# Kernel tuning notes

Hardware: AMD Instinct MI355X
Metric: run time of the kernel (lower is better)

The kernel has to match this reference:

```python
import jax, jax.numpy as jnp
import numpy as np

D_MODEL = 768
NUM_HEADS = 12
HEAD_DIM = D_MODEL // NUM_HEADS

def setup_inputs() -> dict:
    key = jax.random.key(0)
    ks = jax.random.split(key, 7)
    B, S = 2, 4096
    q = jax.random.normal(ks[0], (B, S, D_MODEL), dtype=jnp.float32)
    k = jax.random.normal(ks[1], (B, S, D_MODEL), dtype=jnp.float32)
    v = jax.random.normal(ks[2], (B, S, D_MODEL), dtype=jnp.float32)
    # nn.Linear(d, d, bias=False): weight [out, in], y = x @ W.T
    s = 1.0 / np.sqrt(D_MODEL)
    W_q = jax.random.uniform(ks[3], (D_MODEL, D_MODEL), jnp.float32, -s, s)
    W_k = jax.random.uniform(ks[4], (D_MODEL, D_MODEL), jnp.float32, -s, s)
    W_v = jax.random.uniform(ks[5], (D_MODEL, D_MODEL), jnp.float32, -s, s)
    W_o = jax.random.uniform(ks[6], (D_MODEL, D_MODEL), jnp.float32, -s, s)
    return {"query": q, "key": k, "value": v,
            "W_q": W_q, "W_k": W_k, "W_v": W_v, "W_o": W_o}

def reference(query, key, value, W_q, W_k, W_v, W_o):
    B, S, _ = query.shape
    H, Dh = NUM_HEADS, HEAD_DIM
    scale = np.sqrt(Dh).astype(np.float32)

    def proj(x, W):  # x [B,S,D] -> [B,H,S,Dh]
        y = jnp.einsum('bsd,ed->bse', x, W)
        return y.reshape(B, S, H, Dh).transpose(0, 2, 1, 3)

    Q = proj(query, W_q)
    K = proj(key, W_k)
    V = proj(value, W_v)
    scores = jnp.einsum('bhqd,bhkd->bhqk', Q, K) / scale
    attn = jax.nn.softmax(scores, axis=-1)  # dropout p=0 -> identity (eval)
    out = jnp.einsum('bhqk,bhkd->bhqd', attn, V)
    out = out.transpose(0, 2, 1, 3).reshape(B, S, H * Dh)
    return jnp.einsum('bsd,ed->bse', out, W_o)
```

## Files before the change

### kernel.cpp

```cpp
#include <hip/hip_runtime.h>

#define D_MODEL 768
#define S_LEN   4096
#define NHEAD   12
#define HDIM    64
#define BATCH   2
#define M_ROWS  (BATCH * S_LEN)

typedef __bf16    bf16x8 __attribute__((ext_vector_type(8)));
typedef float     f32x4  __attribute__((ext_vector_type(4)));
typedef float     f32x16 __attribute__((ext_vector_type(16)));
typedef unsigned  u32x4  __attribute__((ext_vector_type(4)));

#define QSCALE 0.18033688011f

__device__ __forceinline__ unsigned int bfb(float x) {
    return (unsigned int)__builtin_bit_cast(unsigned short, (__bf16)x);
}

__device__ __forceinline__ unsigned cvtpk(float lo, float hi) {
    unsigned r;
    asm("v_cvt_pk_bf16_f32 %0, %1, %2" : "=v"(r) : "v"(lo), "v"(hi));
    return r;
}

__device__ __forceinline__ void gload16(const void* g, const void* l) {
    __builtin_amdgcn_global_load_lds(
        (const __attribute__((address_space(1))) unsigned int*)g,
        (__attribute__((address_space(3))) unsigned int*)l, 16, 0, 0);
}

#define MFMA16(a, b, c) __builtin_amdgcn_mfma_f32_16x16x32_bf16(a, b, c, 0, 0, 0)
#define MFMA32(a, b, c) __builtin_amdgcn_mfma_f32_32x32x16_bf16(a, b, c, 0, 0, 0)

__global__ __launch_bounds__(256)
void cvt_bf16(const float* __restrict__ s0, const float* __restrict__ s1,
              const float* __restrict__ s2, const float* __restrict__ s3,
              __bf16* __restrict__ d0, __bf16* __restrict__ d1,
              __bf16* __restrict__ d2, __bf16* __restrict__ d3, int n) {
    const int z = blockIdx.y;
    const float* s = z == 0 ? s0 : z == 1 ? s1 : z == 2 ? s2 : s3;
    __bf16*      d = z == 0 ? d0 : z == 1 ? d1 : z == 2 ? d2 : d3;
    const size_t i = ((size_t)blockIdx.x * 256 + threadIdx.x) * 8;
    if (i >= (size_t)n) return;
    float4 a = *(const float4*)(s + i);
    float4 b = *(const float4*)(s + i + 4);
    bf16x8 o;
    o[0] = (__bf16)a.x; o[1] = (__bf16)a.y; o[2] = (__bf16)a.z; o[3] = (__bf16)a.w;
    o[4] = (__bf16)b.x; o[5] = (__bf16)b.y; o[6] = (__bf16)b.z; o[7] = (__bf16)b.w;
    *(bf16x8*)(d + i) = o;
}

template <int MODE>
__global__ __launch_bounds__(256)
void mm_bf16(const __bf16* __restrict__ Xb, const __bf16* __restrict__ Wb,
             void* __restrict__ C0) {
    __shared__ __align__(16) char lds[16384];
    const int t    = threadIdx.x;
    const int w    = t >> 6;
    const int wr   = w >> 1, wc = w & 1;
    const int lane = t & 63;
    const int q15  = lane & 15;
    const int g    = lane >> 4;
    const int n0   = blockIdx.x * 128;
    const int m0   = blockIdx.y * 128;

    f32x4 acc[4][4];
#pragma unroll
    for (int i = 0; i < 4; i++)
#pragma unroll
        for (int j = 0; j < 4; j++) acc[i][j] = (f32x4){0.f, 0.f, 0.f, 0.f};

    const int srow  = lane >> 2;
    const int sslot = lane & 3;

    for (int k0 = 0; k0 < D_MODEL; k0 += 32) {
        __syncthreads();
#pragma unroll
        for (int j = 0; j < 2; j++) {
            const int lrow = j * 64 + w * 16 + srow;
            const int xs   = (lrow ^ (lrow >> 2)) & 3;
            gload16(Xb + (size_t)(m0 + lrow) * D_MODEL + k0 + ((sslot ^ xs) << 3),
                    lds + j * 4096 + w * 1024);
        }
#pragma unroll
        for (int j = 0; j < 2; j++) {
            const int lrow = j * 64 + w * 16 + srow;
            const int xs   = (lrow ^ (lrow >> 2)) & 3;
            gload16(Wb + (size_t)(n0 + lrow) * D_MODEL + k0 + ((sslot ^ xs) << 3),
                    lds + 8192 + j * 4096 + w * 1024);
        }
        __syncthreads();

        bf16x8 xa[4], wf[4];
#pragma unroll
        for (int mi = 0; mi < 4; mi++) {
            const int r  = wr * 64 + mi * 16 + q15;
            const int sl = g ^ ((r ^ (r >> 2)) & 3);
            xa[mi] = *(const bf16x8*)(lds + r * 64 + sl * 16);
        }
#pragma unroll
        for (int nj = 0; nj < 4; nj++) {
            const int r  = wc * 64 + nj * 16 + q15;
            const int sl = g ^ ((r ^ (r >> 2)) & 3);
            wf[nj] = *(const bf16x8*)(lds + 8192 + r * 64 + sl * 16);
        }
#pragma unroll
        for (int mi = 0; mi < 4; mi++)
#pragma unroll
            for (int nj = 0; nj < 4; nj++)
                acc[mi][nj] = MFMA16(xa[mi], wf[nj], acc[mi][nj]);
    }

#pragma unroll
    for (int mi = 0; mi < 4; mi++) {
#pragma unroll
        for (int nj = 0; nj < 4; nj++) {
            const int n  = n0 + wc * 64 + nj * 16 + q15;
            const int mb = m0 + wr * 64 + mi * 16 + 4 * g;
            if (MODE == 0) {
#pragma unroll
                for (int r = 0; r < 4; r++)
                    ((float*)C0)[(size_t)(mb + r) * D_MODEL + n] = acc[mi][nj][r];
            } else if (MODE == 1) {
                const int h = n >> 6, dh = n & 63;
#pragma unroll
                for (int r = 0; r < 4; r++) {
                    const int m = mb + r, b = m >> 12, s = m & 4095;
                    ((__bf16*)C0)[(((size_t)(b * NHEAD + h)) * S_LEN + s) * HDIM + dh] =
                        (__bf16)(acc[mi][nj][r] * QSCALE);
                }
            } else if (MODE == 2) {
                const int h = n >> 6, dh = n & 63;
#pragma unroll
                for (int r = 0; r < 4; r++) {
                    const int m = mb + r, b = m >> 12, s = m & 4095;
                    ((__bf16*)C0)[(((size_t)(b * NHEAD + h)) * S_LEN + s) * HDIM + dh] =
                        (__bf16)acc[mi][nj][r];
                }
            } else {
                const int h = n >> 6, dh = n & 63;
                const int b = mb >> 12, s = mb & 4095;
                uint2 pk;
                pk.x = bfb(acc[mi][nj][0]) | (bfb(acc[mi][nj][1]) << 16);
                pk.y = bfb(acc[mi][nj][2]) | (bfb(acc[mi][nj][3]) << 16);
                *(uint2*)((__bf16*)C0 +
                    (((size_t)(b * NHEAD + h)) * HDIM + dh) * S_LEN + s) = pk;
            }
        }
    }
}

__global__ __launch_bounds__(256, 2)
void flash_attn(const __bf16* __restrict__ Qb, const char* __restrict__ Kb,
                const char* __restrict__ Vtb, __bf16* __restrict__ Ab) {
    __shared__ __align__(16) char lds[32768];
    const int t    = threadIdx.x;
    const int w    = t >> 6;
    const int lane = t & 63;
    const int q31  = lane & 31;
    const int hl   = lane >> 5;
    const int swz  = (q31 & 7) << 4;

    const int bid = blockIdx.x;
    const int sb  = (bid & 7) * 96 + (bid >> 3);
    const int bh  = sb >> 5;
    const int qi  = sb & 31;
    const int b   = bh / NHEAD, h = bh % NHEAD;
    const int q0  = qi * 128 + w * 32;

    const char* kbase = Kb  + (size_t)bh * (S_LEN * HDIM * 2);
    const char* vbase = Vtb + (size_t)bh * (HDIM * S_LEN * 2);

    bf16x8 qf[4];
#pragma unroll
    for (int kc = 0; kc < 4; kc++)
        qf[kc] = *(const bf16x8*)(Qb +
            ((size_t)bh * S_LEN + q0 + q31) * HDIM + kc * 16 + hl * 8);

    f32x16 o[2];
#pragma unroll
    for (int mt = 0; mt < 2; mt++)
#pragma unroll
        for (int r = 0; r < 16; r++) o[mt][r] = 0.f;
    float lrun = 0.f;

    const int crow = lane >> 3;
    const int scb  = ((lane & 7) << 4) ^ (crow << 4);

#define STAGE(BASE, KT)                                                        \
    {                                                                          \
        _Pragma("unroll")                                                      \
        for (int j = 0; j < 2; j++) {                                          \
            const int c = 2 * w + j;                                           \
            gload16(kbase + (size_t)((KT) * 64 + c * 8 + crow) * 128 + scb,    \
                    (BASE) + c * 1024);                                        \
            gload16(vbase + (size_t)(c * 8 + crow) * (S_LEN * 2) +             \
                        (size_t)(KT) * 128 + scb,                              \
                    (BASE) + 8192 + c * 1024);                                 \
        }                                                                      \
    }

#define COMPUTE(BASE)                                                          \
    {                                                                          \
        const char* Kt = (BASE);                                               \
        const char* Vt = (BASE) + 8192;                                        \
        f32x16 sA[2];                                                          \
        _Pragma("unroll")                                                      \
        for (int mt = 0; mt < 2; mt++)                                         \
            _Pragma("unroll")                                                  \
            for (int r = 0; r < 16; r++) sA[mt][r] = 0.f;                      \
        _Pragma("unroll")                                                      \
        for (int kc = 0; kc < 4; kc++) {                                       \
            bf16x8 kf0 = *(const bf16x8*)(Kt + q31 * 128 +                     \
                                          ((32 * kc + 16 * hl) ^ swz));        \
            bf16x8 kf1 = *(const bf16x8*)(Kt + (32 + q31) * 128 +              \
                                          ((32 * kc + 16 * hl) ^ swz));        \
            sA[0] = MFMA32(kf0, qf[kc], sA[0]);                                \
            sA[1] = MFMA32(kf1, qf[kc], sA[1]);                                \
        }                                                                      \
        float ps = 0.f;                                                        \
        _Pragma("unroll")                                                      \
        for (int mt = 0; mt < 2; mt++)                                         \
            _Pragma("unroll")                                                  \
            for (int r = 0; r < 16; r++) {                                     \
                const float p = exp2f(sA[mt][r]);                              \
                sA[mt][r] = p;                                                 \
                ps += p;                                                       \
            }                                                                  \
        ps += __shfl_xor(ps, 32);                                              \
        lrun += ps;                                                            \
        u32x4 pf[4];                                                           \
        _Pragma("unroll")                                                      \
        for (int mt = 0; mt < 2; mt++)                                         \
            _Pragma("unroll")                                                  \
            for (int kvc = 0; kvc < 2; kvc++) {                                \
                unsigned w0 = cvtpk(sA[mt][8*kvc+0], sA[mt][8*kvc+1]);         \
                unsigned w1 = cvtpk(sA[mt][8*kvc+2], sA[mt][8*kvc+3]);         \
                unsigned w2 = cvtpk(sA[mt][8*kvc+4], sA[mt][8*kvc+5]);         \
                unsigned w3 = cvtpk(sA[mt][8*kvc+6], sA[mt][8*kvc+7]);         \
                asm volatile("v_permlane32_swap_b32 %0, %1"                    \
                             : "+v"(w0), "+v"(w2));                            \
                asm volatile("v_permlane32_swap_b32 %0, %1"                    \
                             : "+v"(w1), "+v"(w3));                            \
                pf[mt * 2 + kvc] = (u32x4){w0, w1, w2, w3};                    \
            }                                                                  \
        _Pragma("unroll")                                                      \
        for (int mtd = 0; mtd < 2; mtd++)                                      \
            _Pragma("unroll")                                                  \
            for (int ks = 0; ks < 4; ks++) {                                   \
                bf16x8 vf = *(const bf16x8*)(Vt + (32 * mtd + q31) * 128 +     \
                                             ((32 * ks + 16 * hl) ^ swz));     \
                o[mtd] = MFMA32(vf,                                            \
                    __builtin_bit_cast(bf16x8, pf[ks]), o[mtd]);               \
            }                                                                  \
    }

    STAGE(lds, 0);
    __syncthreads();
#pragma unroll 1
    for (int kt = 0; kt < S_LEN / 64; kt += 2) {
        STAGE(lds + 16384, kt + 1);
        COMPUTE(lds);
        __syncthreads();
        if (kt + 2 < S_LEN / 64) STAGE(lds, kt + 2);
        COMPUTE(lds + 16384);
        __syncthreads();
    }
#undef STAGE
#undef COMPUTE

    const float inv  = 1.0f / lrun;
    const int   qrow = q0 + q31;
    __bf16* orow = Ab + ((size_t)b * S_LEN + qrow) * D_MODEL + h * HDIM;
#pragma unroll
    for (int mtd = 0; mtd < 2; mtd++)
#pragma unroll
        for (int rg = 0; rg < 4; rg++) {
            const int d0 = 32 * mtd + 8 * rg + 4 * hl;
            uint2 pk;
            pk.x = cvtpk(o[mtd][rg * 4 + 0] * inv, o[mtd][rg * 4 + 1] * inv);
            pk.y = cvtpk(o[mtd][rg * 4 + 2] * inv, o[mtd][rg * 4 + 3] * inv);
            *(uint2*)(orow + d0) = pk;
        }
}

extern "C" void kernel_launch(void* const* d_in, const int* in_sizes, int n_in,
                              void* d_out, int out_size, void* d_ws, size_t ws_size,
                              hipStream_t stream) {
    const float* q  = (const float*)d_in[0];
    const float* k  = (const float*)d_in[1];
    const float* v  = (const float*)d_in[2];
    const float* Wq = (const float*)d_in[3];
    const float* Wk = (const float*)d_in[4];
    const float* Wv = (const float*)d_in[5];
    const float* Wo = (const float*)d_in[6];
    float* out = (float*)d_out;

    const size_t per = (size_t)M_ROWS * D_MODEL;
    const size_t wsz = (size_t)D_MODEL * D_MODEL;
    __bf16* ws  = (__bf16*)d_ws;
    __bf16* qb  = ws;
    __bf16* kb  = qb  + per;
    __bf16* vb  = kb  + per;
    __bf16* Wqb = vb  + per;
    __bf16* Wkb = Wqb + wsz;
    __bf16* Wvb = Wkb + wsz;
    __bf16* Wob = Wvb + wsz;
    __bf16* Qhi = Wob + wsz;
    __bf16* Kbb = Qhi + per;
    __bf16* Vtb = Kbb + per;

    cvt_bf16<<<dim3((int)(per / 2048), 3), 256, 0, stream>>>(
        q, k, v, nullptr, qb, kb, vb, nullptr, (int)per);
    cvt_bf16<<<dim3((int)(wsz / 2048), 4), 256, 0, stream>>>(
        Wq, Wk, Wv, Wo, Wqb, Wkb, Wvb, Wob, (int)wsz);

    dim3 mmg(D_MODEL / 128, M_ROWS / 128);
    mm_bf16<1><<<mmg, 256, 0, stream>>>(qb, Wqb, Qhi);
    mm_bf16<2><<<mmg, 256, 0, stream>>>(kb, Wkb, Kbb);
    mm_bf16<3><<<mmg, 256, 0, stream>>>(vb, Wvb, Vtb);

    flash_attn<<<768, 256, 0, stream>>>(Qhi, (const char*)Kbb,
                                        (const char*)Vtb, qb );

    mm_bf16<0><<<mmg, 256, 0, stream>>>(qb, Wob, out);
}
```

Baseline: 261.4 us.

## Batch QKV projections into one launch and offload softmax row-sum to MFMA

Merges the three Q/K/V projection GEMM launches into a single grid with a z dimension that selects the input and output layout. In flash attention, the per-tile scalar exp2 sum and cross-lane shuffle are replaced by an extra MFMA against a vector of ones, which accumulates the softmax denominator on the matrix units. exp2f is swapped for the native hardware exp2 builtin, and s_setprio hints are wrapped around the MFMA sections. The goal is less launch overhead and fewer VALU instructions in the attention inner loop, at the cost of four extra MFMAs per tile and a 16-register accumulator.

```diff
diff --git a/kernel.cpp b/kernel.cpp
--- a/kernel.cpp
+++ b/kernel.cpp
@@ -22,6 +22,17 @@
     unsigned r;
     asm("v_cvt_pk_bf16_f32 %0, %1, %2" : "=v"(r) : "v"(lo), "v"(hi));
     return r;
+}
+
+#if !__has_builtin(__builtin_amdgcn_exp2f)
+extern "C" __device__ float __ocml_native_exp2_f32(float);
+#endif
+__device__ __forceinline__ float fexp2(float x) {
+#if __has_builtin(__builtin_amdgcn_exp2f)
+    return __builtin_amdgcn_exp2f(x);
+#else
+    return __ocml_native_exp2_f32(x);
+#endif
 }
 
 __device__ __forceinline__ void gload16(const void* g, const void* l) {
@@ -51,10 +62,109 @@
     *(bf16x8*)(d + i) = o;
 }
 
-template <int MODE>
 __global__ __launch_bounds__(256)
-void mm_bf16(const __bf16* __restrict__ Xb, const __bf16* __restrict__ Wb,
-             void* __restrict__ C0) {
+void mm_qkv(const __bf16* __restrict__ X0, const __bf16* __restrict__ X1,
+            const __bf16* __restrict__ X2, const __bf16* __restrict__ W0,
+            const __bf16* __restrict__ W1, const __bf16* __restrict__ W2,
+            __bf16* __restrict__ C0q, __bf16* __restrict__ C1k,
+            __bf16* __restrict__ C2v) {
+    __shared__ __align__(16) char lds[16384];
+    const int z = blockIdx.z;
+    const __bf16* Xb = z == 0 ? X0 : z == 1 ? X1 : X2;
+    const __bf16* Wb = z == 0 ? W0 : z == 1 ? W1 : W2;
+
+    const int t    = threadIdx.x;
+    const int w    = t >> 6;
+    const int wr   = w >> 1, wc = w & 1;
+    const int lane = t & 63;
+    const int q15  = lane & 15;
+    const int g    = lane >> 4;
+    const int n0   = blockIdx.x * 128;
+    const int m0   = blockIdx.y * 128;
+
+    f32x4 acc[4][4];
+#pragma unroll
+    for (int i = 0; i < 4; i++)
+#pragma unroll
+        for (int j = 0; j < 4; j++) acc[i][j] = (f32x4){0.f, 0.f, 0.f, 0.f};
+
+    const int srow  = lane >> 2;
+    const int sslot = lane & 3;
+
+    for (int k0 = 0; k0 < D_MODEL; k0 += 32) {
+        __syncthreads();
+#pragma unroll
+        for (int j = 0; j < 2; j++) {
+            const int lrow = j * 64 + w * 16 + srow;
+            const int xs   = (lrow ^ (lrow >> 2)) & 3;
+            gload16(Xb + (size_t)(m0 + lrow) * D_MODEL + k0 + ((sslot ^ xs) << 3),
+                    lds + j * 4096 + w * 1024);
+        }
+#pragma unroll
+        for (int j = 0; j < 2; j++) {
+            const int lrow = j * 64 + w * 16 + srow;
+            const int xs   = (lrow ^ (lrow >> 2)) & 3;
+            gload16(Wb + (size_t)(n0 + lrow) * D_MODEL + k0 + ((sslot ^ xs) << 3),
+                    lds + 8192 + j * 4096 + w * 1024);
+        }
+        __syncthreads();
+
+        bf16x8 xa[4], wf[4];
+#pragma unroll
+        for (int mi = 0; mi < 4; mi++) {
+            const int r  = wr * 64 + mi * 16 + q15;
+            const int sl = g ^ ((r ^ (r >> 2)) & 3);
+            xa[mi] = *(const bf16x8*)(lds + r * 64 + sl * 16);
+        }
+#pragma unroll
+        for (int nj = 0; nj < 4; nj++) {
+            const int r  = wc * 64 + nj * 16 + q15;
+            const int sl = g ^ ((r ^ (r >> 2)) & 3);
+            wf[nj] = *(const bf16x8*)(lds + 8192 + r * 64 + sl * 16);
+        }
+#pragma unroll
+        for (int mi = 0; mi < 4; mi++)
+#pragma unroll
+            for (int nj = 0; nj < 4; nj++)
+                acc[mi][nj] = MFMA16(xa[mi], wf[nj], acc[mi][nj]);
+    }
+
+#pragma unroll
+    for (int mi = 0; mi < 4; mi++) {
+#pragma unroll
+        for (int nj = 0; nj < 4; nj++) {
+            const int n  = n0 + wc * 64 + nj * 16 + q15;
+            const int mb = m0 + wr * 64 + mi * 16 + 4 * g;
+            const int h = n >> 6, dh = n & 63;
+            if (z == 0) {
+#pragma unroll
+                for (int r = 0; r < 4; r++) {
+                    const int m = mb + r, b = m >> 12, s = m & 4095;
+                    C0q[(((size_t)(b * NHEAD + h)) * S_LEN + s) * HDIM + dh] =
+                        (__bf16)(acc[mi][nj][r] * QSCALE);
+                }
+            } else if (z == 1) {
+#pragma unroll
+                for (int r = 0; r < 4; r++) {
+                    const int m = mb + r, b = m >> 12, s = m & 4095;
+                    C1k[(((size_t)(b * NHEAD + h)) * S_LEN + s) * HDIM + dh] =
+                        (__bf16)acc[mi][nj][r];
+                }
+            } else {
+                const int b = mb >> 12, s = mb & 4095;
+                uint2 pk;
+                pk.x = bfb(acc[mi][nj][0]) | (bfb(acc[mi][nj][1]) << 16);
+                pk.y = bfb(acc[mi][nj][2]) | (bfb(acc[mi][nj][3]) << 16);
+                *(uint2*)(C2v +
+                    (((size_t)(b * NHEAD + h)) * HDIM + dh) * S_LEN + s) = pk;
+            }
+        }
+    }
+}
+
+__global__ __launch_bounds__(256)
+void mm_out(const __bf16* __restrict__ Xb, const __bf16* __restrict__ Wb,
+            float* __restrict__ C0) {
     __shared__ __align__(16) char lds[16384];
     const int t    = threadIdx.x;
     const int w    = t >> 6;
@@ -113,42 +223,15 @@
     }
 
 #pragma unroll
-    for (int mi = 0; mi < 4; mi++) {
+    for (int mi = 0; mi < 4; mi++)
 #pragma unroll
         for (int nj = 0; nj < 4; nj++) {
             const int n  = n0 + wc * 64 + nj * 16 + q15;
             const int mb = m0 + wr * 64 + mi * 16 + 4 * g;
-            if (MODE == 0) {
-#pragma unroll
-                for (int r = 0; r < 4; r++)
-                    ((float*)C0)[(size_t)(mb + r) * D_MODEL + n] = acc[mi][nj][r];
-            } else if (MODE == 1) {
-                const int h = n >> 6, dh = n & 63;
-#pragma unroll
-                for (int r = 0; r < 4; r++) {
-                    const int m = mb + r, b = m >> 12, s = m & 4095;
-                    ((__bf16*)C0)[(((size_t)(b * NHEAD + h)) * S_LEN + s) * HDIM + dh] =
-                        (__bf16)(acc[mi][nj][r] * QSCALE);
-                }
-            } else if (MODE == 2) {
-                const int h = n >> 6, dh = n & 63;
-#pragma unroll
-                for (int r = 0; r < 4; r++) {
-                    const int m = mb + r, b = m >> 12, s = m & 4095;
-                    ((__bf16*)C0)[(((size_t)(b * NHEAD + h)) * S_LEN + s) * HDIM + dh] =
-                        (__bf16)acc[mi][nj][r];
-                }
-            } else {
-                const int h = n >> 6, dh = n & 63;
-                const int b = mb >> 12, s = mb & 4095;
-                uint2 pk;
-                pk.x = bfb(acc[mi][nj][0]) | (bfb(acc[mi][nj][1]) << 16);
-                pk.y = bfb(acc[mi][nj][2]) | (bfb(acc[mi][nj][3]) << 16);
-                *(uint2*)((__bf16*)C0 +
-                    (((size_t)(b * NHEAD + h)) * HDIM + dh) * S_LEN + s) = pk;
-            }
-        }
-    }
+#pragma unroll
+            for (int r = 0; r < 4; r++)
+                C0[(size_t)(mb + r) * D_MODEL + n] = acc[mi][nj][r];
+        }
 }
 
 __global__ __launch_bounds__(256, 2)
@@ -178,12 +261,16 @@
         qf[kc] = *(const bf16x8*)(Qb +
             ((size_t)bh * S_LEN + q0 + q31) * HDIM + kc * 16 + hl * 8);
 
-    f32x16 o[2];
+    const bf16x8 onesv = __builtin_bit_cast(bf16x8,
+        (u32x4){0x3F803F80u, 0x3F803F80u, 0x3F803F80u, 0x3F803F80u});
+
+    f32x16 o[2], ol;
 #pragma unroll
     for (int mt = 0; mt < 2; mt++)
 #pragma unroll
         for (int r = 0; r < 16; r++) o[mt][r] = 0.f;
-    float lrun = 0.f;
+#pragma unroll
+    for (int r = 0; r < 16; r++) ol[r] = 0.f;
 
     const int crow = lane >> 3;
     const int scb  = ((lane & 7) << 4) ^ (crow << 4);
@@ -210,6 +297,7 @@
         for (int mt = 0; mt < 2; mt++)                                         \
             _Pragma("unroll")                                                  \
             for (int r = 0; r < 16; r++) sA[mt][r] = 0.f;                      \
+        __builtin_amdgcn_s_setprio(1);                                         \
         _Pragma("unroll")                                                      \
         for (int kc = 0; kc < 4; kc++) {                                       \
             bf16x8 kf0 = *(const bf16x8*)(Kt + q31 * 128 +                     \
@@ -219,17 +307,11 @@
             sA[0] = MFMA32(kf0, qf[kc], sA[0]);                                \
             sA[1] = MFMA32(kf1, qf[kc], sA[1]);                                \
         }                                                                      \
-        float ps = 0.f;                                                        \
+        __builtin_amdgcn_s_setprio(0);                                         \
         _Pragma("unroll")                                                      \
         for (int mt = 0; mt < 2; mt++)                                         \
             _Pragma("unroll")                                                  \
-            for (int r = 0; r < 16; r++) {                                     \
-                const float p = exp2f(sA[mt][r]);                              \
-                sA[mt][r] = p;                                                 \
-                ps += p;                                                       \
-            }                                                                  \
-        ps += __shfl_xor(ps, 32);                                              \
-        lrun += ps;                                                            \
+            for (int r = 0; r < 16; r++) sA[mt][r] = fexp2(sA[mt][r]);         \
         u32x4 pf[4];                                                           \
         _Pragma("unroll")                                                      \
         for (int mt = 0; mt < 2; mt++)                                         \
@@ -245,6 +327,10 @@
                              : "+v"(w1), "+v"(w3));                            \
                 pf[mt * 2 + kvc] = (u32x4){w0, w1, w2, w3};                    \
             }                                                                  \
+        __builtin_amdgcn_s_setprio(1);                                         \
+        _Pragma("unroll")                                                      \
+        for (int ks = 0; ks < 4; ks++)                                         \
+            ol = MFMA32(onesv, __builtin_bit_cast(bf16x8, pf[ks]), ol);        \
         _Pragma("unroll")                                                      \
         for (int mtd = 0; mtd < 2; mtd++)                                      \
             _Pragma("unroll")                                                  \
@@ -254,6 +340,7 @@
                 o[mtd] = MFMA32(vf,                                            \
                     __builtin_bit_cast(bf16x8, pf[ks]), o[mtd]);               \
             }                                                                  \
+        __builtin_amdgcn_s_setprio(0);                                         \
     }
 
     STAGE(lds, 0);
@@ -270,7 +357,7 @@
 #undef STAGE
 #undef COMPUTE
 
-    const float inv  = 1.0f / lrun;
+    const float inv  = 1.0f / ol[0];
     const int   qrow = q0 + q31;
     __bf16* orow = Ab + ((size_t)b * S_LEN + qrow) * D_MODEL + h * HDIM;
 #pragma unroll
@@ -316,13 +403,12 @@
     cvt_bf16<<<dim3((int)(wsz / 2048), 4), 256, 0, stream>>>(
         Wq, Wk, Wv, Wo, Wqb, Wkb, Wvb, Wob, (int)wsz);
 
-    dim3 mmg(D_MODEL / 128, M_ROWS / 128);
-    mm_bf16<1><<<mmg, 256, 0, stream>>>(qb, Wqb, Qhi);
-    mm_bf16<2><<<mmg, 256, 0, stream>>>(kb, Wkb, Kbb);
-    mm_bf16<3><<<mmg, 256, 0, stream>>>(vb, Wvb, Vtb);
+    dim3 mmg(D_MODEL / 128, M_ROWS / 128, 3);
+    mm_qkv<<<mmg, 256, 0, stream>>>(qb, kb, vb, Wqb, Wkb, Wvb, Qhi, Kbb, Vtb);
 
     flash_attn<<<768, 256, 0, stream>>>(Qhi, (const char*)Kbb,
                                         (const char*)Vtb, qb );
 
-    mm_bf16<0><<<mmg, 256, 0, stream>>>(qb, Wob, out);
-}
+    dim3 mmo(D_MODEL / 128, M_ROWS / 128);
+    mm_out<<<mmo, 256, 0, stream>>>(qb, Wob, out);
+}
```

Measured after the change: 222.5 us. 14.9% less time.
